# Performance work log

Measured on AMD Instinct MI355X. Metric: run time of the kernel, lower is better.

Reference implementation:

```python
import jax, jax.numpy as jnp
import numpy as np
from jax import lax

KH, KW, PAD = 3, 3, 1
K = KH * KW


def _bilinear(x, py, px):
    # x: [B,C,H,W]; py,px: [B,K,H,W] float sample coords; zero outside bounds
    B, C, H, W = x.shape
    y0f = jnp.floor(py); x0f = jnp.floor(px)
    wy = (py - y0f)[:, None]; wx = (px - x0f)[:, None]
    y0 = y0f.astype(jnp.int32); x0 = x0f.astype(jnp.int32)
    xf = x.reshape(B, C, H * W)

    def gather(yi, xi):
        inb = (yi >= 0) & (yi < H) & (xi >= 0) & (xi < W)
        idx = (jnp.clip(yi, 0, H - 1) * W + jnp.clip(xi, 0, W - 1)).reshape(B, -1)
        g = jax.vmap(lambda a, i: a[:, i])(xf, idx).reshape(B, C, K, H, W)
        return g * inb[:, None]

    v00 = gather(y0, x0); v01 = gather(y0, x0 + 1)
    v10 = gather(y0 + 1, x0); v11 = gather(y0 + 1, x0 + 1)
    return (v00 * (1 - wy) * (1 - wx) + v01 * (1 - wy) * wx
            + v10 * wy * (1 - wx) + v11 * wy * wx)


def _mdconv(x, w, ow, ob):
    # ModulatedDeformConvPack (DCNv2): a plain conv predicts offsets (2K ch)
    # and mask (K ch, sigmoid); then modulated bilinear-gather deform conv.
    B, Cin, H, W = x.shape
    off = lax.conv_general_dilated(x, ow, (1, 1), [(PAD, PAD), (PAD, PAD)],
                                   dimension_numbers=('NCHW', 'OIHW', 'NCHW'))
    off = off + ob[None, :, None, None]  # [B,3K,H,W]
    # cat(o1,o2) channels read pairwise: ch 2k -> dy_k, ch 2k+1 -> dx_k
    o12 = jnp.concatenate([off[:, :K], off[:, K:2 * K]], axis=1).reshape(B, K, 2, H, W)
    mask = jax.nn.sigmoid(off[:, 2 * K:])  # [B,K,H,W]
    ki, kj = jnp.meshgrid(jnp.arange(KH), jnp.arange(KW), indexing='ij')
    base_y = (ki.reshape(K)[:, None, None] - PAD + jnp.arange(H)[None, :, None]).astype(x.dtype)
    base_x = (kj.reshape(K)[:, None, None] - PAD + jnp.arange(W)[None, None, :]).astype(x.dtype)
    py = base_y[None] + o12[:, :, 0]  # [B,K,H,W]
    px = base_x[None] + o12[:, :, 1]
    sampled = _bilinear(x, py, px) * mask[:, None]  # [B,Cin,K,H,W]
    return jnp.einsum('bckhw,ock->bohw', sampled, w.reshape(w.shape[0], Cin, K))


def setup_inputs() -> dict:
    key = jax.random.key(0)
    ks = jax.random.split(key, 40)
    B, Cin, Cout, H, W = 8, 64, 64, 64, 64
    d = {}
    d['in_tensor'] = jax.random.normal(ks[0], (B, Cin, H, W), jnp.float32)
    d['last_hidden_state'] = jax.random.normal(ks[1], (B, Cout, H, W), jnp.float32)
    d['last_cell_out'] = jax.random.normal(ks[2], (B, Cout, H, W), jnp.float32)
    for i in range(8):
        cin = Cin if i % 2 == 0 else Cout  # conv1/3/5/7 eat input, conv2/4/6/8 eat hidden
        d[f'w{i+1}'] = jax.random.normal(ks[3 + i], (Cout, cin, KH, KW), jnp.float32) * (1.0 / np.sqrt(cin * K)).astype(np.float32)
        d[f'ow{i+1}'] = jax.random.normal(ks[11 + i], (3 * K, cin, KH, KW), jnp.float32) * 0.01
        d[f'ob{i+1}'] = jax.random.normal(ks[19 + i], (3 * K,), jnp.float32) * 0.01
    for j, name in enumerate(['bi', 'bf', 'bc', 'bo', 'wci', 'wcf', 'wco']):
        d[name] = jax.random.normal(ks[27 + j], (1, Cout, 1, 1), jnp.float32) * 0.05
    return d


def reference(in_tensor, last_hidden_state, last_cell_out,
              w1, w2, w3, w4, w5, w6, w7, w8,
              ow1, ow2, ow3, ow4, ow5, ow6, ow7, ow8,
              ob1, ob2, ob3, ob4, ob5, ob6, ob7, ob8,
              bi, bf, bc, bo, wci, wcf, wco):
    x, h, c = in_tensor, last_hidden_state, last_cell_out
    i_g = jax.nn.sigmoid(_mdconv(x, w1, ow1, ob1) + _mdconv(h, w2, ow2, ob2) + c * wci + bi)
    f_g = jax.nn.sigmoid(_mdconv(x, w3, ow3, ob3) + _mdconv(h, w4, ow4, ob4) + c * wcf + bf)
    c_new = f_g * c + i_g * jnp.tanh(_mdconv(x, w5, ow5, ob5) + _mdconv(h, w6, ow6, ob6) + bc)
    o_g = jax.nn.sigmoid(_mdconv(x, w7, ow7, ob7) + _mdconv(h, w8, ow8, ob8) + c_new * wco + bo)
    h_new = o_g * jnp.tanh(c_new)
    return (h_new, c_new)
```

## Files before the change

### kernel.cpp

```cpp
#include <hip/hip_runtime.h>
#include <math.h>

#define NB     8
#define NC     64
#define HW     4096
#define PLANE  2097152

#define WS_WB     0
#define WS_OWB    147456
#define WS_OB     221184
#define WS_GATES  221400
#define WS_XT     8610008
#define WS_HT     9658584

typedef __bf16 bf16x8 __attribute__((ext_vector_type(8)));
typedef float  f32x4  __attribute__((ext_vector_type(4)));

struct Params {
    const float* x; const float* h; const float* c;
    const float* w[8]; const float* ow[8]; const float* ob[8];
    const float* bi; const float* bf; const float* bc; const float* bo;
    const float* wci; const float* wcf; const float* wco;
    float* out; float* ws;
};

__device__ __forceinline__ float sigf(float v) { return 1.f / (1.f + __expf(-v)); }
__device__ __forceinline__ float tanhfast(float v) {
    return 1.f - 2.f / (__expf(2.f * v) + 1.f);
}
__device__ __forceinline__ unsigned short f2bf(float v) {
    __bf16 b = (__bf16)v;
    return __builtin_bit_cast(unsigned short, b);
}
__device__ __forceinline__ float blo(unsigned d) { return __builtin_bit_cast(float, d << 16); }
__device__ __forceinline__ float bhi(unsigned d) { return __builtin_bit_cast(float, d & 0xffff0000u); }

__global__ __launch_bounds__(256) void k0_prep(Params p) {
    if (blockIdx.x < 1729) {
        int i = blockIdx.x * 256 + threadIdx.x;
        unsigned short* wb  = (unsigned short*)(p.ws + WS_WB);
        unsigned short* owb = (unsigned short*)(p.ws + WS_OWB);
        if (i < 294912) {
            int br = i / 36864; int r = i % 36864;
            int kgrp = r >> 9; int o = (r >> 3) & 63; int j = r & 7;
            int k = kgrp * 8 + j;
            int ktap = k >> 6; int c = k & 63;
            wb[i] = f2bf(p.w[br][(o * 64 + c) * 9 + ktap]);
        } else if (i < 294912 + 147456) {
            int ii = i - 294912;
            int br = ii / 18432; int r = ii % 18432;
            int kgrp = r >> 8; int o = (r >> 3) & 31; int j = r & 7;
            int k = kgrp * 8 + j;
            int ktap = k >> 6; int c = k & 63;
            float v = (o < 27) ? p.ow[br][(o * 64 + c) * 9 + ktap] : 0.f;
            owb[ii] = f2bf(v);
        } else if (i < 294912 + 147456 + 216) {
            int ii = i - 442368;
            int br = ii / 27; int j = ii % 27;
            p.ws[WS_OB + ii] = p.ob[br][j];
        }
        return;
    }
    __shared__ float tile[64][65];
    int bid = blockIdx.x - 1729;
    int row = bid & 63; int b = (bid >> 6) & 7; int ten = bid >> 9;
    const float* src = ten ? p.h : p.x;
    unsigned short* dst = (unsigned short*)(p.ws + (ten ? WS_HT : WS_XT));
    int t = threadIdx.x; int lane = t & 63; int w4 = t >> 6;
#pragma unroll
    for (int i = 0; i < 16; ++i) {
        int c = i * 4 + w4;
        tile[c][lane] = src[((size_t)(b * 64 + c) << 12) + row * 64 + lane];
    }
    __syncthreads();
#pragma unroll
    for (int i = 0; i < 16; ++i) {
        int px = i * 4 + w4;
        dst[((size_t)(b * 4096 + row * 64 + px) << 6) + lane] = f2bf(tile[lane][px]);
    }
}

__global__ __launch_bounds__(256, 2) void k2_fused(Params p) {
    __shared__ __align__(16) unsigned char arena[63232];
    uint2*  sA   = (uint2*)(arena + 40960);
    float4* sWp  = (float4*)(arena + 45568);
    float*  sOff = (float*)(arena + 54784);

    int bid = blockIdx.x;
    int b = bid & 7; int gate = (bid >> 3) & 3; int row = bid >> 5;
    int t = threadIdx.x; int l = t & 63; int w = t >> 6;
    int q = l >> 4; int n = l & 15;
    int pxl = w * 16 + n;

    const unsigned short* wBp = (const unsigned short*)(p.ws + WS_WB);
    const unsigned short* owb = (const unsigned short*)(p.ws + WS_OWB);

    int qb = q * 16 - (row - 2) * 8192;

    f32x4 acc[4];
#pragma unroll
    for (int ot = 0; ot < 4; ++ot) acc[ot] = (f32x4){0.f, 0.f, 0.f, 0.f};

    for (int sub = 0; sub < 2; ++sub) {
        int br = gate * 2 + sub;
        const unsigned short* inT =
            (const unsigned short*)(p.ws + (sub ? WS_HT : WS_XT)) + ((size_t)b << 18);
        const float* obp = p.ws + WS_OB + br * 27;

        __syncthreads();
#pragma unroll
        for (int it = 0; it < 10; ++it) {
            int u = t + it * 256;
            int r = u >> 9; int px = (u >> 3) & 63; int seg = u & 7;
            int grow = row - 2 + r;
            uint4 v = {0u, 0u, 0u, 0u};
            if ((unsigned)grow < 64u)
                v = *(const uint4*)(inT + (((size_t)grow * 64 + px) << 6) + seg * 8);
            unsigned byte = ((unsigned)u << 4) ^ (((unsigned)px & 7u) << 4);
            *(uint4*)(arena + byte) = v;
        }
        __syncthreads();

        auto loadA_oc = [&](int u) -> bf16x8 {
            int dy = u / 6; int s = u - dy * 6;
            int spx = w * 16 + n + (s >> 1) - 1;
            int spc = min(max(spx, 0), 63);
            int cgb = (s & 1) * 4 + q;
            unsigned byte = ((unsigned)(((dy + 1) * 64 + spc) << 7) + cgb * 16)
                            ^ (((unsigned)spc & 7u) << 4);
            bf16x8 af = *(const bf16x8*)(arena + byte);
            if ((unsigned)spx >= 64u) {
#pragma unroll
                for (int z = 0; z < 8; ++z) af[z] = (__bf16)0.f;
            }
            return af;
        };
        auto loadB_oc = [&](int u, int ot) -> bf16x8 {
            int dy = u / 6; int s = u - dy * 6;
            int kb = (br * 72 + dy * 24 + s * 4 + q) * 32;
            return *(const bf16x8*)(owb + (size_t)(kb + ot * 16 + n) * 8);
        };
        f32x4 a2c0 = (f32x4){0.f,0.f,0.f,0.f}, a2c1 = (f32x4){0.f,0.f,0.f,0.f};
        f32x4 a2c2 = (f32x4){0.f,0.f,0.f,0.f}, a2c3 = (f32x4){0.f,0.f,0.f,0.f};
        bf16x8 eA = loadA_oc(0), eB0 = loadB_oc(0, 0), eB1 = loadB_oc(0, 1);
        bf16x8 dA = loadA_oc(1), dB0 = loadB_oc(1, 0), dB1 = loadB_oc(1, 1);
#pragma unroll 1
        for (int u2 = 0; u2 < 9; ++u2) {
            bf16x8 neA = eA, neB0 = eB0, neB1 = eB1;
            bf16x8 ndA = dA, ndB0 = dB0, ndB1 = dB1;
            if (u2 < 8) {
                neA = loadA_oc(2 * u2 + 2); neB0 = loadB_oc(2 * u2 + 2, 0); neB1 = loadB_oc(2 * u2 + 2, 1);
                ndA = loadA_oc(2 * u2 + 3); ndB0 = loadB_oc(2 * u2 + 3, 0); ndB1 = loadB_oc(2 * u2 + 3, 1);
            }
            a2c0 = __builtin_amdgcn_mfma_f32_16x16x32_bf16(eA, eB0, a2c0, 0, 0, 0);
            a2c1 = __builtin_amdgcn_mfma_f32_16x16x32_bf16(eA, eB1, a2c1, 0, 0, 0);
            a2c2 = __builtin_amdgcn_mfma_f32_16x16x32_bf16(dA, dB0, a2c2, 0, 0, 0);
            a2c3 = __builtin_amdgcn_mfma_f32_16x16x32_bf16(dA, dB1, a2c3, 0, 0, 0);
            eA = neA; eB0 = neB0; eB1 = neB1;
            dA = ndA; dB0 = ndB0; dB1 = ndB1;
        }
        f32x4 acc2[2];
        acc2[0] = a2c0 + a2c2;
        acc2[1] = a2c1 + a2c3;

#pragma unroll
        for (int ot = 0; ot < 2; ++ot) {
            int j = ot * 16 + n;
            float bias = (j < 27) ? obp[j] : 0.f;
#pragma unroll
            for (int r = 0; r < 4; ++r)
                sOff[j * 66 + w * 16 + q * 4 + r] = acc2[ot][r] + bias;
        }
        __syncthreads();

        for (int i2 = t; i2 < 576; i2 += 256) {
            int px = i2 & 63; int k = i2 >> 6;
            float dy = sOff[(2 * k) * 66 + px];
            float dx = sOff[(2 * k + 1) * 66 + px];
            float mm = sOff[(18 + k) * 66 + px];
            float m = sigf(mm);
            int ki = k / 3, kj = k % 3;
            float py  = (float)(row + ki - 1) + dy;
            float pxx = (float)(px + kj - 1) + dx;
            float y0f = floorf(py), x0f = floorf(pxx);
            float wy = py - y0f, wx = pxx - x0f;
            int y0 = (int)y0f, x0 = (int)x0f;
            float y0i = ((unsigned)y0 < 64u) ? 1.f : 0.f;
            float y1i = ((unsigned)(y0 + 1) < 64u) ? 1.f : 0.f;
            float x0i = ((unsigned)x0 < 64u) ? 1.f : 0.f;
            float x1i = ((unsigned)(x0 + 1) < 64u) ? 1.f : 0.f;
            float w00 = (1.f - wy) * (1.f - wx) * m * y0i * x0i;
            float w01 = (1.f - wy) * wx         * m * y0i * x1i;
            float w10 = wy         * (1.f - wx) * m * y1i * x0i;
            float w11 = wy         * wx         * m * y1i * x1i;
            int cy0 = min(max(y0, 0), 63),     cy1 = min(max(y0 + 1, 0), 63);
            int cx0 = min(max(x0, 0), 63),     cx1 = min(max(x0 + 1, 0), 63);
            int s0 = cy0 - (row - 2); int s1 = cy1 - (row - 2);
            unsigned farb = (((unsigned)s0 > 4u) || ((unsigned)s1 > 4u)) ? 0x80000000u : 0u;
            sA[k * 64 + px] = make_uint2(((unsigned)(cy0 * 64 + cx0) | ((unsigned)(cy0 * 64 + cx1) << 16)) | farb,
                                         (unsigned)(cy1 * 64 + cx0) | ((unsigned)(cy1 * 64 + cx1) << 16));
            sWp[k * 64 + px] = make_float4(w00, w01, w10, w11);
        }
        __syncthreads();

        const unsigned short* cbase = inT + q * 8;
        auto loadB_mn = [&](int S, int ot) -> bf16x8 {
            int kb = (br * 72 + S * 4 + q) * 64;
            return *(const bf16x8*)(wBp + (size_t)(kb + ot * 16 + n) * 8);
        };

#define PROC(Ca, Cb, Cc, Cd, WV, Wa, Wb, Wc, Wd)                               \
        {                                                                      \
            float sacc[8];                                                     \
            sacc[0] = WV.x * blo(Ca.x); sacc[1] = WV.x * bhi(Ca.x);            \
            sacc[2] = WV.x * blo(Ca.y); sacc[3] = WV.x * bhi(Ca.y);            \
            sacc[4] = WV.x * blo(Ca.z); sacc[5] = WV.x * bhi(Ca.z);            \
            sacc[6] = WV.x * blo(Ca.w); sacc[7] = WV.x * bhi(Ca.w);            \
            sacc[0] += WV.y * blo(Cb.x); sacc[1] += WV.y * bhi(Cb.x);          \
            sacc[2] += WV.y * blo(Cb.y); sacc[3] += WV.y * bhi(Cb.y);          \
            sacc[4] += WV.y * blo(Cb.z); sacc[5] += WV.y * bhi(Cb.z);          \
            sacc[6] += WV.y * blo(Cb.w); sacc[7] += WV.y * bhi(Cb.w);          \
            sacc[0] += WV.z * blo(Cc.x); sacc[1] += WV.z * bhi(Cc.x);          \
            sacc[2] += WV.z * blo(Cc.y); sacc[3] += WV.z * bhi(Cc.y);          \
            sacc[4] += WV.z * blo(Cc.z); sacc[5] += WV.z * bhi(Cc.z);          \
            sacc[6] += WV.z * blo(Cc.w); sacc[7] += WV.z * bhi(Cc.w);          \
            sacc[0] += WV.w * blo(Cd.x); sacc[1] += WV.w * bhi(Cd.x);          \
            sacc[2] += WV.w * blo(Cd.y); sacc[3] += WV.w * bhi(Cd.y);          \
            sacc[4] += WV.w * blo(Cd.z); sacc[5] += WV.w * bhi(Cd.z);          \
            sacc[6] += WV.w * blo(Cd.w); sacc[7] += WV.w * bhi(Cd.w);          \
            bf16x8 af;                                                         \
            _Pragma("unroll")                                                  \
            for (int j = 0; j < 8; ++j) af[j] = (__bf16)sacc[j];               \
            acc[0] = __builtin_amdgcn_mfma_f32_16x16x32_bf16(af, Wa, acc[0], 0, 0, 0); \
            acc[1] = __builtin_amdgcn_mfma_f32_16x16x32_bf16(af, Wb, acc[1], 0, 0, 0); \
            acc[2] = __builtin_amdgcn_mfma_f32_16x16x32_bf16(af, Wc, acc[2], 0, 0, 0); \
            acc[3] = __builtin_amdgcn_mfma_f32_16x16x32_bf16(af, Wd, acc[3], 0, 0, 0); \
        }

        uint2 aa = sA[pxl];
        float4 wv = sWp[pxl];
        unsigned p00 = aa.x & 0xFFFu, p01 = (aa.x >> 16) & 0xFFFu;
        unsigned p10 = aa.y & 0xFFFu, p11 = aa.y >> 16;
        unsigned a00 = (unsigned)(((int)(p00 << 7)) + qb) ^ ((p00 & 7u) << 4);
        unsigned a01 = (unsigned)(((int)(p01 << 7)) + qb) ^ ((p01 & 7u) << 4);
        unsigned a10 = (unsigned)(((int)(p10 << 7)) + qb) ^ ((p10 & 7u) << 4);
        unsigned a11 = (unsigned)(((int)(p11 << 7)) + qb) ^ ((p11 & 7u) << 4);
        uint4 C0a = *(const uint4*)(arena + a00);
        uint4 C0b = *(const uint4*)(arena + a01);
        uint4 C0c = *(const uint4*)(arena + a10);
        uint4 C0d = *(const uint4*)(arena + a11);
        uint4 C1a = *(const uint4*)(arena + (a00 ^ 64u));
        uint4 C1b = *(const uint4*)(arena + (a01 ^ 64u));
        uint4 C1c = *(const uint4*)(arena + (a10 ^ 64u));
        uint4 C1d = *(const uint4*)(arena + (a11 ^ 64u));
        if (aa.x & 0x80000000u) {
            C0a = *(const uint4*)(cbase + (p00 << 6));
            C0b = *(const uint4*)(cbase + (p01 << 6));
            C0c = *(const uint4*)(cbase + (p10 << 6));
            C0d = *(const uint4*)(cbase + (p11 << 6));
            C1a = *(const uint4*)(cbase + (p00 << 6) + 32);
            C1b = *(const uint4*)(cbase + (p01 << 6) + 32);
            C1c = *(const uint4*)(cbase + (p10 << 6) + 32);
            C1d = *(const uint4*)(cbase + (p11 << 6) + 32);
        }
        bf16x8 B0a = loadB_mn(0, 0), B0b = loadB_mn(0, 1), B0c = loadB_mn(0, 2), B0d = loadB_mn(0, 3);
        bf16x8 B1a = loadB_mn(1, 0), B1b = loadB_mn(1, 1), B1c = loadB_mn(1, 2), B1d = loadB_mn(1, 3);
#pragma unroll 1
        for (int ktap = 0; ktap < 9; ++ktap) {
            uint4 N0a = C0a, N0b = C0b, N0c = C0c, N0d = C0d;
            uint4 N1a = C1a, N1b = C1b, N1c = C1c, N1d = C1d;
            float4 wvn = wv;
            bf16x8 nB0a = B0a, nB0b = B0b, nB0c = B0c, nB0d = B0d;
            bf16x8 nB1a = B1a, nB1b = B1b, nB1c = B1c, nB1d = B1d;
            if (ktap < 8) {
                uint2 aan = sA[(ktap + 1) * 64 + pxl];
                wvn = sWp[(ktap + 1) * 64 + pxl];
                unsigned q00 = aan.x & 0xFFFu, q01 = (aan.x >> 16) & 0xFFFu;
                unsigned q10 = aan.y & 0xFFFu, q11 = aan.y >> 16;
                unsigned b00 = (unsigned)(((int)(q00 << 7)) + qb) ^ ((q00 & 7u) << 4);
                unsigned b01 = (unsigned)(((int)(q01 << 7)) + qb) ^ ((q01 & 7u) << 4);
                unsigned b10 = (unsigned)(((int)(q10 << 7)) + qb) ^ ((q10 & 7u) << 4);
                unsigned b11 = (unsigned)(((int)(q11 << 7)) + qb) ^ ((q11 & 7u) << 4);
                N0a = *(const uint4*)(arena + b00);
                N0b = *(const uint4*)(arena + b01);
                N0c = *(const uint4*)(arena + b10);
                N0d = *(const uint4*)(arena + b11);
                N1a = *(const uint4*)(arena + (b00 ^ 64u));
                N1b = *(const uint4*)(arena + (b01 ^ 64u));
                N1c = *(const uint4*)(arena + (b10 ^ 64u));
                N1d = *(const uint4*)(arena + (b11 ^ 64u));
                if (aan.x & 0x80000000u) {
                    N0a = *(const uint4*)(cbase + (q00 << 6));
                    N0b = *(const uint4*)(cbase + (q01 << 6));
                    N0c = *(const uint4*)(cbase + (q10 << 6));
                    N0d = *(const uint4*)(cbase + (q11 << 6));
                    N1a = *(const uint4*)(cbase + (q00 << 6) + 32);
                    N1b = *(const uint4*)(cbase + (q01 << 6) + 32);
                    N1c = *(const uint4*)(cbase + (q10 << 6) + 32);
                    N1d = *(const uint4*)(cbase + (q11 << 6) + 32);
                }
                nB0a = loadB_mn(2 * ktap + 2, 0); nB0b = loadB_mn(2 * ktap + 2, 1);
                nB0c = loadB_mn(2 * ktap + 2, 2); nB0d = loadB_mn(2 * ktap + 2, 3);
                nB1a = loadB_mn(2 * ktap + 3, 0); nB1b = loadB_mn(2 * ktap + 3, 1);
                nB1c = loadB_mn(2 * ktap + 3, 2); nB1d = loadB_mn(2 * ktap + 3, 3);
            }
            PROC(C0a, C0b, C0c, C0d, wv, B0a, B0b, B0c, B0d)
            PROC(C1a, C1b, C1c, C1d, wv, B1a, B1b, B1c, B1d)
            C0a = N0a; C0b = N0b; C0c = N0c; C0d = N0d;
            C1a = N1a; C1b = N1b; C1c = N1c; C1d = N1d;
            B0a = nB0a; B0b = nB0b; B0c = nB0c; B0d = nB0d;
            B1a = nB1a; B1b = nB1b; B1c = nB1c; B1d = nB1d;
            wv = wvn;
        }
#undef PROC
    }

    float* gp = p.ws + WS_GATES + ((size_t)((gate * 8 + b) * 64 + row) << 12);
#pragma unroll
    for (int ot = 0; ot < 4; ++ot)
        *(float4*)(gp + ((w * 4 + ot) * 64 + l) * 4) = *(float4*)&acc[ot];
}

__global__ __launch_bounds__(256) void k3_lstm(Params p) {
    int T = blockIdx.x * 256 + threadIdx.x;
    int i = T & 4095; int row = (T >> 12) & 63; int b = T >> 18;
    const float* gp = p.ws + WS_GATES;
    size_t base = ((size_t)(b * 64 + row) << 12) + i;
    float gi = gp[base];
    float gf = gp[base + 1 * PLANE];
    float gc = gp[base + 2 * PLANE];
    float go = gp[base + 3 * PLANE];
    int r = i & 3; int l = (i >> 2) & 63; int u = i >> 8;
    int w = u >> 2; int ot = u & 3;
    int o = ot * 16 + (l & 15);
    int px = w * 16 + (l >> 4) * 4 + r;
    size_t cidx = ((size_t)(b * 64 + o) << 12) + row * 64 + px;
    float cold = p.c[cidx];
    float ig = sigf(gi + cold * p.wci[o] + p.bi[o]);
    float fg = sigf(gf + cold * p.wcf[o] + p.bf[o]);
    float cn = fg * cold + ig * tanhfast(gc + p.bc[o]);
    float og = sigf(go + cn * p.wco[o] + p.bo[o]);
    p.out[cidx] = og * tanhfast(cn);
    p.out[cidx + PLANE] = cn;
}

extern "C" void kernel_launch(void* const* d_in, const int* in_sizes, int n_in,
                              void* d_out, int out_size, void* d_ws, size_t ws_size,
                              hipStream_t stream) {
    (void)in_sizes; (void)n_in; (void)out_size; (void)ws_size;
    Params P;
    P.x = (const float*)d_in[0];
    P.h = (const float*)d_in[1];
    P.c = (const float*)d_in[2];
    for (int i = 0; i < 8; ++i) {
        P.w[i]  = (const float*)d_in[3 + 3 * i];
        P.ow[i] = (const float*)d_in[4 + 3 * i];
        P.ob[i] = (const float*)d_in[5 + 3 * i];
    }
    P.bi  = (const float*)d_in[27];
    P.bf  = (const float*)d_in[28];
    P.bc  = (const float*)d_in[29];
    P.bo  = (const float*)d_in[30];
    P.wci = (const float*)d_in[31];
    P.wcf = (const float*)d_in[32];
    P.wco = (const float*)d_in[33];
    P.out = (float*)d_out;
    P.ws  = (float*)d_ws;

    k0_prep   <<<dim3(2753), dim3(256), 0, stream>>>(P);
    k2_fused  <<<dim3(2048), dim3(256), 0, stream>>>(P);
    k3_lstm   <<<dim3(8192), dim3(256), 0, stream>>>(P);
}
```

Before: 274.6 us.

## Shrink LDS footprint to fit three blocks per CU

Stores the bilinear sample weights as fp16 instead of fp32 and aliases the offset scratch buffer onto the index/weight region. The offsets are read into registers behind an extra barrier first. LDS per block drops from about 63KB to 50KB, and launch bounds ask for 3 blocks per CU to hide gather latency. The fp16 weights lose some precision, and tighter register limits could cause spills.

After: 380.9 us. 38.7% more time.

```diff
diff --git a/kernel.cpp b/kernel.cpp
--- a/kernel.cpp
+++ b/kernel.cpp
@@ -15,6 +15,7 @@
 
 typedef __bf16 bf16x8 __attribute__((ext_vector_type(8)));
 typedef float  f32x4  __attribute__((ext_vector_type(4)));
+typedef _Float16 f16x4 __attribute__((ext_vector_type(4)));
 
 struct Params {
     const float* x; const float* h; const float* c;
@@ -80,11 +81,11 @@
     }
 }
 
-__global__ __launch_bounds__(256, 2) void k2_fused(Params p) {
-    __shared__ __align__(16) unsigned char arena[63232];
-    uint2*  sA   = (uint2*)(arena + 40960);
-    float4* sWp  = (float4*)(arena + 45568);
-    float*  sOff = (float*)(arena + 54784);
+__global__ __launch_bounds__(256, 3) void k2_fused(Params p) {
+    __shared__ __align__(16) unsigned char arena[50176];
+    uint2* sA   = (uint2*)(arena + 40960);
+    f16x4* sWp  = (f16x4*)(arena + 45568);
+    float* sOff = (float*)(arena + 40960);
 
     int bid = blockIdx.x;
     int b = bid & 7; int gate = (bid >> 3) & 3; int row = bid >> 5;
@@ -123,7 +124,7 @@
 
         auto loadA_oc = [&](int u) -> bf16x8 {
             int dy = u / 6; int s = u - dy * 6;
-            int spx = w * 16 + n + (s >> 1) - 1;
+            int spx = pxl + (s >> 1) - 1;
             int spc = min(max(spx, 0), 63);
             int cgb = (s & 1) * 4 + q;
             unsigned byte = ((unsigned)(((dy + 1) * 64 + spc) << 7) + cgb * 16)
@@ -140,8 +141,8 @@
             int kb = (br * 72 + dy * 24 + s * 4 + q) * 32;
             return *(const bf16x8*)(owb + (size_t)(kb + ot * 16 + n) * 8);
         };
-        f32x4 a2c0 = (f32x4){0.f,0.f,0.f,0.f}, a2c1 = (f32x4){0.f,0.f,0.f,0.f};
-        f32x4 a2c2 = (f32x4){0.f,0.f,0.f,0.f}, a2c3 = (f32x4){0.f,0.f,0.f,0.f};
+        f32x4 c0 = (f32x4){0.f,0.f,0.f,0.f}, c1 = (f32x4){0.f,0.f,0.f,0.f};
+        f32x4 c2 = (f32x4){0.f,0.f,0.f,0.f}, c3 = (f32x4){0.f,0.f,0.f,0.f};
         bf16x8 eA = loadA_oc(0), eB0 = loadB_oc(0, 0), eB1 = loadB_oc(0, 1);
         bf16x8 dA = loadA_oc(1), dB0 = loadB_oc(1, 0), dB1 = loadB_oc(1, 1);
 #pragma unroll 1
@@ -152,32 +153,49 @@
                 neA = loadA_oc(2 * u2 + 2); neB0 = loadB_oc(2 * u2 + 2, 0); neB1 = loadB_oc(2 * u2 + 2, 1);
                 ndA = loadA_oc(2 * u2 + 3); ndB0 = loadB_oc(2 * u2 + 3, 0); ndB1 = loadB_oc(2 * u2 + 3, 1);
             }
-            a2c0 = __builtin_amdgcn_mfma_f32_16x16x32_bf16(eA, eB0, a2c0, 0, 0, 0);
-            a2c1 = __builtin_amdgcn_mfma_f32_16x16x32_bf16(eA, eB1, a2c1, 0, 0, 0);
-            a2c2 = __builtin_amdgcn_mfma_f32_16x16x32_bf16(dA, dB0, a2c2, 0, 0, 0);
-            a2c3 = __builtin_amdgcn_mfma_f32_16x16x32_bf16(dA, dB1, a2c3, 0, 0, 0);
+            c0 = __builtin_amdgcn_mfma_f32_16x16x32_bf16(eA, eB0, c0, 0, 0, 0);
+            c1 = __builtin_amdgcn_mfma_f32_16x16x32_bf16(eA, eB1, c1, 0, 0, 0);
+            c2 = __builtin_amdgcn_mfma_f32_16x16x32_bf16(dA, dB0, c2, 0, 0, 0);
+            c3 = __builtin_amdgcn_mfma_f32_16x16x32_bf16(dA, dB1, c3, 0, 0, 0);
             eA = neA; eB0 = neB0; eB1 = neB1;
             dA = ndA; dB0 = ndB0; dB1 = ndB1;
         }
         f32x4 acc2[2];
-        acc2[0] = a2c0 + a2c2;
-        acc2[1] = a2c1 + a2c3;
+        acc2[0] = c0 + c2;
+        acc2[1] = c1 + c3;
 
 #pragma unroll
         for (int ot = 0; ot < 2; ++ot) {
             int j = ot * 16 + n;
-            float bias = (j < 27) ? obp[j] : 0.f;
-#pragma unroll
-            for (int r = 0; r < 4; ++r)
-                sOff[j * 66 + w * 16 + q * 4 + r] = acc2[ot][r] + bias;
-        }
-        __syncthreads();
-
-        for (int i2 = t; i2 < 576; i2 += 256) {
+            if (j < 27) {
+                float bias = obp[j];
+#pragma unroll
+                for (int r = 0; r < 4; ++r)
+                    sOff[j * 66 + w * 16 + q * 4 + r] = acc2[ot][r] + bias;
+            }
+        }
+        __syncthreads();
+
+        int iA = t, iB = t + 256, iC = t + 512;
+        float ady, adx, amm, bdy, bdx, bmm;
+        float cdy = 0.f, cdx = 0.f, cmm = 0.f;
+        {
+            int px = iA & 63, k = iA >> 6;
+            ady = sOff[(2 * k) * 66 + px]; adx = sOff[(2 * k + 1) * 66 + px];
+            amm = sOff[(18 + k) * 66 + px];
+            px = iB & 63; k = iB >> 6;
+            bdy = sOff[(2 * k) * 66 + px]; bdx = sOff[(2 * k + 1) * 66 + px];
+            bmm = sOff[(18 + k) * 66 + px];
+            if (iC < 576) {
+                px = iC & 63; k = iC >> 6;
+                cdy = sOff[(2 * k) * 66 + px]; cdx = sOff[(2 * k + 1) * 66 + px];
+                cmm = sOff[(18 + k) * 66 + px];
+            }
+        }
+        __syncthreads();
+
+        auto phaseA_item = [&](int i2, float dy, float dx, float mm) {
             int px = i2 & 63; int k = i2 >> 6;
-            float dy = sOff[(2 * k) * 66 + px];
-            float dx = sOff[(2 * k + 1) * 66 + px];
-            float mm = sOff[(18 + k) * 66 + px];
             float m = sigf(mm);
             int ki = k / 3, kj = k % 3;
             float py  = (float)(row + ki - 1) + dy;
@@ -199,8 +217,11 @@
             unsigned farb = (((unsigned)s0 > 4u) || ((unsigned)s1 > 4u)) ? 0x80000000u : 0u;
             sA[k * 64 + px] = make_uint2(((unsigned)(cy0 * 64 + cx0) | ((unsigned)(cy0 * 64 + cx1) << 16)) | farb,
                                          (unsigned)(cy1 * 64 + cx0) | ((unsigned)(cy1 * 64 + cx1) << 16));
-            sWp[k * 64 + px] = make_float4(w00, w01, w10, w11);
-        }
+            sWp[k * 64 + px] = (f16x4){(_Float16)w00, (_Float16)w01, (_Float16)w10, (_Float16)w11};
+        };
+        phaseA_item(iA, ady, adx, amm);
+        phaseA_item(iB, bdy, bdx, bmm);
+        if (iC < 576) phaseA_item(iC, cdy, cdx, cmm);
         __syncthreads();
 
         const unsigned short* cbase = inT + q * 8;
@@ -238,7 +259,8 @@
         }
 
         uint2 aa = sA[pxl];
-        float4 wv = sWp[pxl];
+        f16x4 wv4 = sWp[pxl];
+        float4 wv = make_float4((float)wv4[0], (float)wv4[1], (float)wv4[2], (float)wv4[3]);
         unsigned p00 = aa.x & 0xFFFu, p01 = (aa.x >> 16) & 0xFFFu;
         unsigned p10 = aa.y & 0xFFFu, p11 = aa.y >> 16;
         unsigned a00 = (unsigned)(((int)(p00 << 7)) + qb) ^ ((p00 & 7u) << 4);
@@ -274,7 +296,8 @@
             bf16x8 nB1a = B1a, nB1b = B1b, nB1c = B1c, nB1d = B1d;
             if (ktap < 8) {
                 uint2 aan = sA[(ktap + 1) * 64 + pxl];
-                wvn = sWp[(ktap + 1) * 64 + pxl];
+                f16x4 wvn4 = sWp[(ktap + 1) * 64 + pxl];
+                wvn = make_float4((float)wvn4[0], (float)wvn4[1], (float)wvn4[2], (float)wvn4[3]);
                 unsigned q00 = aan.x & 0xFFFu, q01 = (aan.x >> 16) & 0xFFFu;
                 unsigned q10 = aan.y & 0xFFFu, q11 = aan.y >> 16;
                 unsigned b00 = (unsigned)(((int)(q00 << 7)) + qb) ^ ((q00 & 7u) << 4);
```
